# Kernel optimization log

Measured on AMD Instinct MI355X. Metric: run time of the kernel, lower is better.

Reference implementation:

```python
import jax, jax.numpy as jnp
import numpy as np

A = 9               # anchors per location (3 scales x 3 ratios)
STRIDE = 32         # backbone stride 16 * conv1 stride 2
PRE_NMS = 2000      # boxes kept before NMS
POST_NMS = 300      # rois kept after NMS
NMS_THRESH = 0.7
MIN_SIZE = 16.0
NEG = jnp.float32(-1e30)


def _generate_anchors(base_size=16, ratios=(0.5, 1.0, 2.0), scales=(8, 16, 32)):
    xc = yc = 0.5 * (base_size - 1)
    size = float(base_size * base_size)
    anchors = []
    for r in ratios:
        ws = np.round(np.sqrt(size / r))
        hs = np.round(ws * r)
        for s in scales:
            w, h = ws * s, hs * s
            anchors.append([xc - 0.5 * (w - 1), yc - 0.5 * (h - 1),
                            xc + 0.5 * (w - 1), yc + 0.5 * (h - 1)])
    return np.array(anchors, dtype=np.float32)  # [A,4]


def _conv(x, w, b, stride, pad):
    y = jax.lax.conv_general_dilated(
        x, w, (stride, stride), ((pad, pad), (pad, pad)),
        dimension_numbers=('NCHW', 'OIHW', 'NCHW'))
    return y + b[None, :, None, None]


def _iou_matrix(boxes):
    x1, y1, x2, y2 = boxes[:, 0], boxes[:, 1], boxes[:, 2], boxes[:, 3]
    area = (x2 - x1 + 1.0) * (y2 - y1 + 1.0)
    iw = jnp.maximum(0.0, jnp.minimum(x2[:, None], x2[None, :]) - jnp.maximum(x1[:, None], x1[None, :]) + 1.0)
    ih = jnp.maximum(0.0, jnp.minimum(y2[:, None], y2[None, :]) - jnp.maximum(y1[:, None], y1[None, :]) + 1.0)
    inter = iw * ih
    return inter / (area[:, None] + area[None, :] - inter)


def _nms_single(boxes, scores):
    # boxes [K,4] sorted by score desc; scores [K] (NEG = filtered out)
    K = boxes.shape[0]
    iou = _iou_matrix(boxes)
    prio = jnp.arange(K, 0, -1)

    def step(valid, _):
        any_valid = jnp.any(valid)
        pick = jnp.argmax(jnp.where(valid, prio, 0))
        new_valid = valid & (iou[pick] <= NMS_THRESH)
        return new_valid, (pick, any_valid)

    valid0 = scores > NEG * 0.5
    _, (picks, flags) = jax.lax.scan(step, valid0, None, length=POST_NMS)
    sel = boxes[picks] * flags[:, None].astype(boxes.dtype)
    return sel, jnp.sum(flags.astype(jnp.int32))


def _proposal(deltas, scores):
    B, _, H, W = deltas.shape
    im_h, im_w = float(H * STRIDE), float(W * STRIDE)
    anchors = jnp.asarray(_generate_anchors())  # [A,4]
    sx = (jnp.arange(W) * STRIDE).astype(jnp.float32)
    sy = (jnp.arange(H) * STRIDE).astype(jnp.float32)
    gx, gy = jnp.meshgrid(sx, sy)  # [H,W] each
    shift = jnp.stack([gx, gy, gx, gy], axis=-1)  # [H,W,4]
    anc = (shift[:, :, None, :] + anchors[None, None, :, :]).reshape(-1, 4)  # [H*W*A,4]

    d = deltas.reshape(B, A, 4, H, W).transpose(0, 3, 4, 1, 2).reshape(B, -1, 4)  # [B,N,4]
    s = scores[:, A:].transpose(0, 2, 3, 1).reshape(B, -1)  # fg scores [B,N]

    ws = anc[:, 2] - anc[:, 0] + 1.0
    hs = anc[:, 3] - anc[:, 1] + 1.0
    cx = anc[:, 0] + 0.5 * ws
    cy = anc[:, 1] + 0.5 * hs
    pcx = d[:, :, 0] * ws + cx
    pcy = d[:, :, 1] * hs + cy
    pw = jnp.exp(d[:, :, 2]) * ws
    ph = jnp.exp(d[:, :, 3]) * hs
    boxes = jnp.stack([pcx - 0.5 * pw, pcy - 0.5 * ph,
                       pcx + 0.5 * pw, pcy + 0.5 * ph], axis=-1)  # [B,N,4]
    lim = jnp.array([im_w - 1, im_h - 1, im_w - 1, im_h - 1], jnp.float32)
    boxes = jnp.minimum(jnp.maximum(boxes, 0.0), lim)

    bw = boxes[..., 2] - boxes[..., 0] + 1.0
    bh = boxes[..., 3] - boxes[..., 1] + 1.0
    s = jnp.where((bw >= MIN_SIZE) & (bh >= MIN_SIZE), s, NEG)

    top_s, idx = jax.lax.top_k(s, PRE_NMS)  # sorted desc
    top_b = jnp.take_along_axis(boxes, idx[:, :, None], axis=1)  # [B,PRE,4]

    sel, num = jax.vmap(_nms_single)(top_b, top_s)  # [B,POST,4], [B]
    bidx = jnp.broadcast_to(jnp.arange(B, dtype=sel.dtype)[:, None, None], (B, POST_NMS, 1))
    rois = jnp.concatenate([bidx, sel], axis=-1)  # [B,POST,5]
    return rois, num


def setup_inputs() -> dict:
    key = jax.random.key(0)
    k = jax.random.split(key, 4)
    x = jax.random.normal(k[0], (4, 512, 96, 160), jnp.float32)
    w1 = jax.random.normal(k[1], (512, 512, 3, 3), jnp.float32) * 0.02
    b1 = jnp.zeros((512,), jnp.float32)
    w_bbox = jax.random.normal(k[2], (36, 512, 1, 1), jnp.float32) * 0.02
    b_bbox = jnp.zeros((36,), jnp.float32)
    w_cls = jax.random.normal(k[3], (18, 512, 3, 3), jnp.float32) * 0.02
    b_cls = jnp.zeros((18,), jnp.float32)
    return dict(x=x, w1=w1, b1=b1, w_bbox=w_bbox, b_bbox=b_bbox, w_cls=w_cls, b_cls=b_cls)


def reference(x, w1, b1, w_bbox, b_bbox, w_cls, b_cls):
    feat = _conv(x, w1, b1, 2, 1)           # [B,512,H/2,W/2]
    deltas = _conv(feat, w_bbox, b_bbox, 1, 0)  # [B,36,h,w]
    cls = _conv(feat, w_cls, b_cls, 1, 1)       # [B,18,h,w]
    return _proposal(deltas, cls)
```

## Files before the change

kernel.cpp:

```cpp
#include <hip/hip_runtime.h>
#include <stdint.h>

typedef unsigned long long u64;
typedef unsigned int u32;

__constant__ float c_aw[9] = {184.f,368.f,736.f,128.f,256.f,512.f, 88.f,176.f,352.f};
__constant__ float c_ah[9] = { 96.f,192.f,384.f,128.f,256.f,512.f,176.f,352.f,704.f};

__global__ __launch_bounds__(256) void transpose_k(const float* __restrict__ w1,
                                                   float* __restrict__ wt2) {
  int e = blockIdx.x * 256 + threadIdx.x;
  int m = e & 7;
  int t = e >> 3;
  int k = t % 9;
  int r = t / 9;
  int ci = r & 511;
  int g = r >> 9;
  wt2[e] = w1[(size_t)(g * 8 + m) * 4608 + ci * 9 + k];
}

__global__ __launch_bounds__(256, 3) void conv1_k(const float* __restrict__ x,
                                                  const float* __restrict__ wt2,
                                                  const float* __restrict__ b1,
                                                  float* __restrict__ feat) {
  __shared__ float xs[8 * 9 * 164];
  const int tid = threadIdx.x;
  const int lane = tid & 63;
  const int wv = __builtin_amdgcn_readfirstlane(tid >> 6);
  const int owg = lane & 15;
  const int ohl = lane >> 4;
  const int n = blockIdx.z;
  const int gg = blockIdx.x * 4 + wv;
  const int oh0 = blockIdx.y * 4;
  const int ih_base = 2 * oh0 - 1;

  int soff[6], loff[6];
  float okf[6];
  bool act[6];
#pragma unroll
  for (int it = 0; it < 6; ++it) {
    int e2 = tid + 256 * it;
    act[it] = (e2 < 1449);
    int e = act[it] ? e2 : 0;
    int ih = e / 161;
    int c = e - ih * 161;
    int gih = ih_base + ih;
    int giw = c - 1;
    bool ok = act[it] && ((unsigned)gih < 96u) && ((unsigned)giw < 160u);
    int cg = min(max(gih, 0), 95);
    int cw = min(max(giw, 0), 159);
    soff[it] = cg * 160 + cw;
    loff[it] = ih * 164 + c;
    okf[it] = ok ? 1.f : 0.f;
  }

  float acc[8][5];
#pragma unroll
  for (int m = 0; m < 8; ++m)
#pragma unroll
    for (int j = 0; j < 5; ++j) acc[m][j] = 0.f;

  const float* xb = x + (size_t)n * 512 * 96 * 160;
  const float* wgb = wt2 + (size_t)gg * 512 * 72;

  float r[6][8];
#pragma unroll
  for (int it = 0; it < 6; ++it)
#pragma unroll
    for (int ci = 0; ci < 8; ++ci)
      r[it][ci] = xb[(size_t)ci * 15360 + soff[it]];

  for (int c0 = 0; c0 < 512; c0 += 8) {
    __syncthreads();
#pragma unroll
    for (int it = 0; it < 6; ++it) {
      if (act[it]) {
        const float m_ = okf[it];
#pragma unroll
        for (int ci = 0; ci < 8; ++ci)
          xs[loff[it] + ci * 1476] = m_ * r[it][ci];
      }
    }
    __syncthreads();
    if (c0 + 8 < 512) {
      const float* xn = xb + (size_t)(c0 + 8) * 15360;
#pragma unroll
      for (int it = 0; it < 6; ++it)
#pragma unroll
        for (int ci = 0; ci < 8; ++ci)
          r[it][ci] = xn[(size_t)ci * 15360 + soff[it]];
    }

    for (int ci = 0; ci < 8; ++ci) {
      const float* wp = wgb + (size_t)(c0 + ci) * 72;
      const float* xrow = &xs[(ci * 9 + 2 * ohl) * 164 + owg * 10];
#pragma unroll
      for (int kh = 0; kh < 3; ++kh) {
        float xv[12];
        const float* xr = xrow + kh * 164;
#pragma unroll
        for (int t2 = 0; t2 < 6; ++t2) {
          float2 t = *(const float2*)(xr + 2 * t2);
          xv[2 * t2] = t.x; xv[2 * t2 + 1] = t.y;
        }
#pragma unroll
        for (int kw = 0; kw < 3; ++kw) {
          const float* wk = wp + (kh * 3 + kw) * 8;
#pragma unroll
          for (int j = 0; j < 5; ++j) {
            const float xj = xv[kw + 2 * j];
            acc[0][j] += wk[0] * xj; acc[1][j] += wk[1] * xj;
            acc[2][j] += wk[2] * xj; acc[3][j] += wk[3] * xj;
            acc[4][j] += wk[4] * xj; acc[5][j] += wk[5] * xj;
            acc[6][j] += wk[6] * xj; acc[7][j] += wk[7] * xj;
          }
        }
      }
    }
  }
  const int oh = oh0 + ohl;
  const int owb = owg * 5;
#pragma unroll
  for (int m = 0; m < 8; ++m) {
    const int co = gg * 8 + m;
    const float bv = b1[co];
    float* op = &feat[(((size_t)n * 512 + co) * 48 + oh) * 80 + owb];
#pragma unroll
    for (int j = 0; j < 5; ++j) op[j] = acc[m][j] + bv;
  }
}

__global__ __launch_bounds__(256) void heads_k(const float* __restrict__ feat,
                                               const float* __restrict__ wb,
                                               const float* __restrict__ bb,
                                               const float* __restrict__ wcg,
                                               const float* __restrict__ bc,
                                               float* __restrict__ deltas,
                                               float* __restrict__ s) {
  __shared__ float smem[5328];
  const int tid = threadIdx.x;

  if (blockIdx.x < 120) {
    float* fs  = smem;
    float* wsb = smem + 2048;
    const int blk = blockIdx.x;
    const int b = blk / 30;
    const int pos0 = (blk % 30) * 128;
    const int pl = tid >> 1, cg = tid & 1;
    const int cbase = cg * 18;
    float acc[18];
#pragma unroll
    for (int j = 0; j < 18; ++j) acc[j] = 0.f;
    const float* fb = feat + (size_t)b * 512 * 3840;

    for (int c0 = 0; c0 < 512; c0 += 16) {
      for (int e = tid; e < 16 * 128; e += 256)
        fs[e] = fb[(size_t)(c0 + (e >> 7)) * 3840 + pos0 + (e & 127)];
      for (int e = tid; e < 16 * 36; e += 256) {
        int ci = e / 36, c = e - ci * 36;
        wsb[e] = wb[(size_t)c * 512 + c0 + ci];
      }
      __syncthreads();
      for (int ci = 0; ci < 16; ++ci) {
        float xv = fs[ci * 128 + pl];
#pragma unroll
        for (int j = 0; j < 18; ++j) acc[j] += xv * wsb[ci * 36 + cbase + j];
      }
      __syncthreads();
    }
    size_t o = ((size_t)b * 3840 + pos0 + pl) * 36 + cbase;
#pragma unroll
    for (int j = 0; j < 18; ++j) deltas[o + j] = acc[j] + bb[cbase + j];
  } else {
    float (*fs)[3][84] = (float(*)[3][84])smem;
    float (*wc)[9][9]  = (float(*)[9][9])(smem + 4032);
    const int bid2 = blockIdx.x - 120;
    const int oh = bid2 % 48;
    const int b = bid2 / 48;
    const int pos = tid % 80;
    const int cg = tid / 80;
    float acc[3] = {0.f, 0.f, 0.f};
    const float* fb = feat + (size_t)b * 512 * 3840;

    for (int c0 = 0; c0 < 512; c0 += 16) {
      for (int e = tid; e < 16 * 246; e += 256) {
        int ci = e / 246;
        int r = e - ci * 246;
        int ihl = r / 82;
        int iw = r - ihl * 82 - 1;
        int gih = oh - 1 + ihl;
        float v = 0.f;
        if ((unsigned)gih < 48u && (unsigned)iw < 80u)
          v = fb[(size_t)(c0 + ci) * 3840 + gih * 80 + iw];
        fs[ci][ihl][iw + 1] = v;
      }
      for (int e = tid; e < 16 * 81; e += 256) {
        int ci = e / 81;
        int r = e - ci * 81;
        int co = r / 9;
        int k = r - co * 9;
        wc[ci][co][k] = wcg[((size_t)(9 + co) * 512 + c0 + ci) * 9 + k];
      }
      __syncthreads();
      if (cg < 3) {
        const int cb = cg * 3;
        for (int ci = 0; ci < 16; ++ci) {
#pragma unroll
          for (int kh = 0; kh < 3; ++kh) {
#pragma unroll
            for (int kw = 0; kw < 3; ++kw) {
              float xv = fs[ci][kh][pos + kw];
              acc[0] += xv * wc[ci][cb + 0][kh * 3 + kw];
              acc[1] += xv * wc[ci][cb + 1][kh * 3 + kw];
              acc[2] += xv * wc[ci][cb + 2][kh * 3 + kw];
            }
          }
        }
      }
      __syncthreads();
    }
    if (cg < 3) {
      const int cb = cg * 3;
      size_t o = (size_t)b * 34560 + ((size_t)oh * 80 + pos) * 9 + cb;
#pragma unroll
      for (int j = 0; j < 3; ++j) s[o + j] = acc[j] + bc[9 + cb + j];
    }
  }
}

__global__ __launch_bounds__(256) void decode_k(const float* __restrict__ deltas,
                                                const float* __restrict__ s,
                                                float* __restrict__ boxes,
                                                u64* __restrict__ keys) {
  const int g = blockIdx.x * 256 + threadIdx.x;
  const int b = g / 34560;
  const int i = g - b * 34560;
  const int pos = i / 9;
  const int a = i - pos * 9;
  const int h = pos / 80;
  const int w = pos - h * 80;
  const float gx = (float)(w * 32);
  const float gy = (float)(h * 32);
  const float aw = c_aw[a], ah = c_ah[a];
  const float x1a = 7.5f - 0.5f * (aw - 1.f);
  const float y1a = 7.5f - 0.5f * (ah - 1.f);
  const float ws_ = aw, hs_ = ah;
  const float cx = (gx + x1a) + 0.5f * ws_;
  const float cy = (gy + y1a) + 0.5f * hs_;

  const float* dp = &deltas[((size_t)b * 3840 + pos) * 36 + a * 4];
  const float d0 = dp[0], d1 = dp[1], d2 = dp[2], d3 = dp[3];
  const float pcx = __fadd_rn(__fmul_rn(d0, ws_), cx);
  const float pcy = __fadd_rn(__fmul_rn(d1, hs_), cy);
  const float pw = __fmul_rn(expf(d2), ws_);
  const float ph = __fmul_rn(expf(d3), hs_);
  float bx1 = __fsub_rn(pcx, __fmul_rn(0.5f, pw));
  float by1 = __fsub_rn(pcy, __fmul_rn(0.5f, ph));
  float bx2 = __fadd_rn(pcx, __fmul_rn(0.5f, pw));
  float by2 = __fadd_rn(pcy, __fmul_rn(0.5f, ph));
  bx1 = fminf(fmaxf(bx1, 0.f), 2559.f);
  by1 = fminf(fmaxf(by1, 0.f), 1535.f);
  bx2 = fminf(fmaxf(bx2, 0.f), 2559.f);
  by2 = fminf(fmaxf(by2, 0.f), 1535.f);
  const float bw = __fadd_rn(__fsub_rn(bx2, bx1), 1.f);
  const float bh = __fadd_rn(__fsub_rn(by2, by1), 1.f);
  float sc = s[g];
  if (!(bw >= 16.f && bh >= 16.f)) sc = -1e30f;

  float4 bo;
  bo.x = bx1; bo.y = by1; bo.z = bx2; bo.w = by2;
  *(float4*)&boxes[(size_t)g * 4] = bo;

  u32 sb = __float_as_uint(sc);
  u32 ou = (sb & 0x80000000u) ? ~sb : (sb | 0x80000000u);
  keys[g] = ((u64)ou << 32) | (u32)(~(u32)i);
}

__global__ __launch_bounds__(1024) void selcomp_k(const u64* __restrict__ keys,
                                                  u64* __restrict__ sel) {
  __shared__ u32 h[2048];
  __shared__ int s_bin;
  __shared__ u32 s_above;
  __shared__ int sc;
  const int b = blockIdx.x;
  const int tid = threadIdx.x;
  const u64* kb = keys + (size_t)b * 34560;
  u64 prefix = 0, pmask = 0;
  int rank = 2000;

#pragma unroll 1
  for (int pass = 0; pass < 6; ++pass) {
    int shift = 53 - 11 * pass;
    if (shift < 0) shift = 0;
    h[tid] = 0; h[tid + 1024] = 0;
    __syncthreads();
    for (int i = tid; i < 34560; i += 1024) {
      u64 k = kb[i];
      if ((k & pmask) == prefix)
        atomicAdd(&h[(u32)((k >> shift) & 2047ull)], 1u);
    }
    __syncthreads();
    for (int off = 1; off < 2048; off <<= 1) {
      u32 t0, t1;
      { int i = tid;        t0 = h[i] + ((i + off < 2048) ? h[i + off] : 0u); }
      { int i = tid + 1024; t1 = h[i] + ((i + off < 2048) ? h[i + off] : 0u); }
      __syncthreads();
      h[tid] = t0; h[tid + 1024] = t1;
      __syncthreads();
    }
#pragma unroll
    for (int q = 0; q < 2; ++q) {
      int i = tid + 1024 * q;
      u32 Si = h[i];
      u32 Sn = (i < 2047) ? h[i + 1] : 0u;
      if ((int)Si >= rank && (int)Sn < rank) { s_bin = i; s_above = Sn; }
    }
    __syncthreads();
    rank -= (int)s_above;
    prefix |= ((u64)(u32)s_bin) << shift;
    pmask |= (2047ull << shift);
    __syncthreads();
  }
  if (tid == 0) sc = 0;
  __syncthreads();
  for (int i = tid; i < 34560; i += 1024) {
    u64 k = kb[i];
    if (k >= prefix) {
      int p = atomicAdd(&sc, 1);
      sel[(size_t)b * 2048 + p] = k;
    }
  }
}

__global__ __launch_bounds__(1024) void nms2_k(const u64* __restrict__ sel,
                                               const float* __restrict__ boxes,
                                               float* __restrict__ out) {
  __shared__ u64 K[2048];
  __shared__ float bx1[2000], by1[2000], bx2[2000], by2[2000], ar[2000];
  __shared__ unsigned char val[2000];
  __shared__ int s_pick, s_cur, s_cnt;
  const int b = blockIdx.x;
  const int tid = threadIdx.x;

  for (int i = tid; i < 2048; i += 1024)
    K[i] = (i < 2000) ? sel[(size_t)b * 2048 + i] : 0ull;
  __syncthreads();
  for (int k2 = 2; k2 <= 2048; k2 <<= 1) {
    for (int j = k2 >> 1; j > 0; j >>= 1) {
      for (int i = tid; i < 2048; i += 1024) {
        int l = i ^ j;
        if (l > i) {
          u64 a = K[i], c = K[l];
          bool up = ((i & k2) == 0);
          if (up ? (a < c) : (a > c)) { K[i] = c; K[l] = a; }
        }
      }
      __syncthreads();
    }
  }
  for (int i = tid; i < 2000; i += 1024) {
    u64 key = K[i];
    u32 ou = (u32)(key >> 32);
    int idx = (int)(~(u32)key);
    u32 sb = (ou & 0x80000000u) ? (ou & 0x7FFFFFFFu) : ~ou;
    float sc = __uint_as_float(sb);
    const float4 bo = *(const float4*)&boxes[((size_t)b * 34560 + idx) * 4];
    bx1[i] = bo.x; by1[i] = bo.y; bx2[i] = bo.z; by2[i] = bo.w;
    ar[i] = __fmul_rn(__fadd_rn(__fsub_rn(bo.z, bo.x), 1.f),
                      __fadd_rn(__fsub_rn(bo.w, bo.y), 1.f));
    val[i] = (sc > -5e29f) ? 1 : 0;
  }
  if (tid == 0) { s_cur = 0; s_cnt = 0; }
  __syncthreads();

  for (int t = 0; t < 300; ++t) {
    if (tid == 0) {
      int c = s_cur;
      while (c < 2000 && !val[c]) ++c;
      if (c < 2000) { s_pick = c; s_cur = c + 1; s_cnt = t + 1; }
      else s_pick = -1;
    }
    __syncthreads();
    const int p = s_pick;
    if (p < 0) break;
    const float px1 = bx1[p], py1 = by1[p], px2 = bx2[p], py2 = by2[p], pa = ar[p];
    if (tid == 0) {
      float* row = out + ((size_t)b * 300 + t) * 5;
      row[0] = (float)b; row[1] = px1; row[2] = py1; row[3] = px2; row[4] = py2;
    }
    for (int jj = p + 1 + tid; jj < 2000; jj += 1024) {
      if (val[jj]) {
        float iw = __fadd_rn(__fsub_rn(fminf(px2, bx2[jj]), fmaxf(px1, bx1[jj])), 1.f);
        iw = fmaxf(0.f, iw);
        float ih = __fadd_rn(__fsub_rn(fminf(py2, by2[jj]), fmaxf(py1, by1[jj])), 1.f);
        ih = fmaxf(0.f, ih);
        float inter = __fmul_rn(iw, ih);
        float denom = __fsub_rn(__fadd_rn(pa, ar[jj]), inter);
        float iou = __fdiv_rn(inter, denom);
        if (iou > 0.7f) val[jj] = 0;
      }
    }
    __syncthreads();
  }

  __syncthreads();
  const int cnt = s_cnt;
  for (int t = cnt + tid; t < 300; t += 1024) {
    float* row = out + ((size_t)b * 300 + t) * 5;
    row[0] = (float)b; row[1] = 0.f; row[2] = 0.f; row[3] = 0.f; row[4] = 0.f;
  }
  if (tid == 0) out[6000 + b] = (float)cnt;
}

extern "C" void kernel_launch(void* const* d_in, const int* in_sizes, int n_in,
                              void* d_out, int out_size, void* d_ws, size_t ws_size,
                              hipStream_t stream) {
  const float* x  = (const float*)d_in[0];
  const float* w1 = (const float*)d_in[1];
  const float* b1 = (const float*)d_in[2];
  const float* wb = (const float*)d_in[3];
  const float* bb = (const float*)d_in[4];
  const float* wc = (const float*)d_in[5];
  const float* bc = (const float*)d_in[6];
  float* out = (float*)d_out;
  char* ws = (char*)d_ws;

  float* feat   = (float*)(ws + 0);
  float* wt2    = (float*)(ws + 31457280);
  float* deltas = (float*)(ws + 40894464);
  float* s      = (float*)(ws + 43106304);
  float* boxes  = (float*)(ws + 43659264);
  u64*   keys   = (u64*)  (ws + 45871104);
  u64*   sel    = (u64*)  (ws + 46977088);

  hipLaunchKernelGGL(transpose_k, dim3(9216), dim3(256), 0, stream, w1, wt2);
  hipLaunchKernelGGL(conv1_k, dim3(16, 12, 4), dim3(256), 0, stream, x, wt2, b1, feat);
  hipLaunchKernelGGL(heads_k, dim3(312), dim3(256), 0, stream, feat, wb, bb, wc, bc, deltas, s);
  hipLaunchKernelGGL(decode_k, dim3(540), dim3(256), 0, stream, deltas, s, boxes, keys);
  hipLaunchKernelGGL(selcomp_k, dim3(4), dim3(1024), 0, stream, keys, sel);
  hipLaunchKernelGGL(nms2_k, dim3(4), dim3(1024), 0, stream, sel, boxes, out);
}
```

Before: 1.599 ms.

## Double-buffer conv1 LDS tile, privatize selection histograms, shrink NMS block

The conv1 kernel now uses two LDS buffers of 4 input channels each instead of one 8-channel buffer. This lets the next tile be written while the current one is computed, so one barrier per iteration can go. The weight transpose switches to coalesced reads with scattered writes. The radix-select histogram is replicated four ways to cut atomic contention, with an extra reduction step added. The NMS kernel drops from 1024 to 256 threads per block to reduce barrier cost in its serial 300-step loop. The risk is that it also loses parallelism in the bitonic sort and the IoU sweep.

```diff
diff --git a/kernel.cpp b/kernel.cpp
--- a/kernel.cpp
+++ b/kernel.cpp
@@ -10,20 +10,19 @@
 __global__ __launch_bounds__(256) void transpose_k(const float* __restrict__ w1,
                                                    float* __restrict__ wt2) {
   int e = blockIdx.x * 256 + threadIdx.x;
-  int m = e & 7;
-  int t = e >> 3;
-  int k = t % 9;
-  int r = t / 9;
-  int ci = r & 511;
-  int g = r >> 9;
-  wt2[e] = w1[(size_t)(g * 8 + m) * 4608 + ci * 9 + k];
+  int q = e % 4608;
+  int co = e / 4608;
+  int ci = q / 9;
+  int k = q - ci * 9;
+  int g = co >> 3, m = co & 7;
+  wt2[(((size_t)g * 512 + ci) * 9 + k) * 8 + m] = w1[e];
 }
 
 __global__ __launch_bounds__(256, 3) void conv1_k(const float* __restrict__ x,
                                                   const float* __restrict__ wt2,
                                                   const float* __restrict__ b1,
                                                   float* __restrict__ feat) {
-  __shared__ float xs[8 * 9 * 164];
+  __shared__ float xs[2][4 * 9 * 164];
   const int tid = threadIdx.x;
   const int lane = tid & 63;
   const int wv = __builtin_amdgcn_readfirstlane(tid >> 6);
@@ -47,9 +46,7 @@
     int gih = ih_base + ih;
     int giw = c - 1;
     bool ok = act[it] && ((unsigned)gih < 96u) && ((unsigned)giw < 160u);
-    int cg = min(max(gih, 0), 95);
-    int cw = min(max(giw, 0), 159);
-    soff[it] = cg * 160 + cw;
+    soff[it] = min(max(gih, 0), 95) * 160 + min(max(giw, 0), 159);
     loff[it] = ih * 164 + c;
     okf[it] = ok ? 1.f : 0.f;
   }
@@ -63,45 +60,62 @@
   const float* xb = x + (size_t)n * 512 * 96 * 160;
   const float* wgb = wt2 + (size_t)gg * 512 * 72;
 
-  float r[6][8];
+  float r[6][4];
 #pragma unroll
   for (int it = 0; it < 6; ++it)
 #pragma unroll
-    for (int ci = 0; ci < 8; ++ci)
+    for (int ci = 0; ci < 4; ++ci)
       r[it][ci] = xb[(size_t)ci * 15360 + soff[it]];
-
-  for (int c0 = 0; c0 < 512; c0 += 8) {
-    __syncthreads();
-#pragma unroll
-    for (int it = 0; it < 6; ++it) {
-      if (act[it]) {
-        const float m_ = okf[it];
-#pragma unroll
-        for (int ci = 0; ci < 8; ++ci)
-          xs[loff[it] + ci * 1476] = m_ * r[it][ci];
-      }
-    }
-    __syncthreads();
-    if (c0 + 8 < 512) {
-      const float* xn = xb + (size_t)(c0 + 8) * 15360;
+#pragma unroll
+  for (int it = 0; it < 6; ++it) {
+    if (act[it]) {
+      const float m_ = okf[it];
+#pragma unroll
+      for (int ci = 0; ci < 4; ++ci)
+        xs[0][loff[it] + ci * 1476] = m_ * r[it][ci];
+    }
+  }
+#pragma unroll
+  for (int it = 0; it < 6; ++it)
+#pragma unroll
+    for (int ci = 0; ci < 4; ++ci)
+      r[it][ci] = xb[(size_t)(4 + ci) * 15360 + soff[it]];
+
+  for (int t = 0; t < 128; ++t) {
+    __syncthreads();
+    const int cur = t & 1;
+    if (t < 127) {
+#pragma unroll
+      for (int it = 0; it < 6; ++it) {
+        if (act[it]) {
+          const float m_ = okf[it];
+#pragma unroll
+          for (int ci = 0; ci < 4; ++ci)
+            xs[cur ^ 1][loff[it] + ci * 1476] = m_ * r[it][ci];
+        }
+      }
+    }
+    if (t < 126) {
+      const float* xn = xb + (size_t)(t + 2) * 4 * 15360;
 #pragma unroll
       for (int it = 0; it < 6; ++it)
 #pragma unroll
-        for (int ci = 0; ci < 8; ++ci)
+        for (int ci = 0; ci < 4; ++ci)
           r[it][ci] = xn[(size_t)ci * 15360 + soff[it]];
     }
 
-    for (int ci = 0; ci < 8; ++ci) {
+    const int c0 = t * 4;
+    for (int ci = 0; ci < 4; ++ci) {
       const float* wp = wgb + (size_t)(c0 + ci) * 72;
-      const float* xrow = &xs[(ci * 9 + 2 * ohl) * 164 + owg * 10];
+      const float* xrow = &xs[cur][(ci * 9 + 2 * ohl) * 164 + owg * 10];
 #pragma unroll
       for (int kh = 0; kh < 3; ++kh) {
         float xv[12];
         const float* xr = xrow + kh * 164;
 #pragma unroll
         for (int t2 = 0; t2 < 6; ++t2) {
-          float2 t = *(const float2*)(xr + 2 * t2);
-          xv[2 * t2] = t.x; xv[2 * t2 + 1] = t.y;
+          float2 tt = *(const float2*)(xr + 2 * t2);
+          xv[2 * t2] = tt.x; xv[2 * t2 + 1] = tt.y;
         }
 #pragma unroll
         for (int kw = 0; kw < 3; ++kw) {
@@ -278,7 +292,7 @@
 
 __global__ __launch_bounds__(1024) void selcomp_k(const u64* __restrict__ keys,
                                                   u64* __restrict__ sel) {
-  __shared__ u32 h[2048];
+  __shared__ u32 h4[4 * 2048];
   __shared__ int s_bin;
   __shared__ u32 s_above;
   __shared__ int sc;
@@ -287,32 +301,41 @@
   const u64* kb = keys + (size_t)b * 34560;
   u64 prefix = 0, pmask = 0;
   int rank = 2000;
+  const int rep = (tid & 3) * 2048;
 
 #pragma unroll 1
   for (int pass = 0; pass < 6; ++pass) {
     int shift = 53 - 11 * pass;
     if (shift < 0) shift = 0;
-    h[tid] = 0; h[tid + 1024] = 0;
+#pragma unroll
+    for (int q = 0; q < 8; ++q) h4[tid + 1024 * q] = 0;
     __syncthreads();
     for (int i = tid; i < 34560; i += 1024) {
       u64 k = kb[i];
       if ((k & pmask) == prefix)
-        atomicAdd(&h[(u32)((k >> shift) & 2047ull)], 1u);
+        atomicAdd(&h4[rep + (u32)((k >> shift) & 2047ull)], 1u);
+    }
+    __syncthreads();
+    {
+      int i = tid;
+      if (i < 2048) h4[i] += h4[i + 2048] + h4[i + 4096] + h4[i + 6144];
+      i = tid + 1024;
+      if (i < 2048) h4[i] += h4[i + 2048] + h4[i + 4096] + h4[i + 6144];
     }
     __syncthreads();
     for (int off = 1; off < 2048; off <<= 1) {
       u32 t0, t1;
-      { int i = tid;        t0 = h[i] + ((i + off < 2048) ? h[i + off] : 0u); }
-      { int i = tid + 1024; t1 = h[i] + ((i + off < 2048) ? h[i + off] : 0u); }
-      __syncthreads();
-      h[tid] = t0; h[tid + 1024] = t1;
+      { int i = tid;        t0 = h4[i] + ((i + off < 2048) ? h4[i + off] : 0u); }
+      { int i = tid + 1024; t1 = h4[i] + ((i + off < 2048) ? h4[i + off] : 0u); }
+      __syncthreads();
+      h4[tid] = t0; h4[tid + 1024] = t1;
       __syncthreads();
     }
 #pragma unroll
     for (int q = 0; q < 2; ++q) {
       int i = tid + 1024 * q;
-      u32 Si = h[i];
-      u32 Sn = (i < 2047) ? h[i + 1] : 0u;
+      u32 Si = h4[i];
+      u32 Sn = (i < 2047) ? h4[i + 1] : 0u;
       if ((int)Si >= rank && (int)Sn < rank) { s_bin = i; s_above = Sn; }
     }
     __syncthreads();
@@ -332,9 +355,9 @@
   }
 }
 
-__global__ __launch_bounds__(1024) void nms2_k(const u64* __restrict__ sel,
-                                               const float* __restrict__ boxes,
-                                               float* __restrict__ out) {
+__global__ __launch_bounds__(256) void nms2_k(const u64* __restrict__ sel,
+                                              const float* __restrict__ boxes,
+                                              float* __restrict__ out) {
   __shared__ u64 K[2048];
   __shared__ float bx1[2000], by1[2000], bx2[2000], by2[2000], ar[2000];
   __shared__ unsigned char val[2000];
@@ -342,12 +365,12 @@
   const int b = blockIdx.x;
   const int tid = threadIdx.x;
 
-  for (int i = tid; i < 2048; i += 1024)
+  for (int i = tid; i < 2048; i += 256)
     K[i] = (i < 2000) ? sel[(size_t)b * 2048 + i] : 0ull;
   __syncthreads();
   for (int k2 = 2; k2 <= 2048; k2 <<= 1) {
     for (int j = k2 >> 1; j > 0; j >>= 1) {
-      for (int i = tid; i < 2048; i += 1024) {
+      for (int i = tid; i < 2048; i += 256) {
         int l = i ^ j;
         if (l > i) {
           u64 a = K[i], c = K[l];
@@ -358,7 +381,7 @@
       __syncthreads();
     }
   }
-  for (int i = tid; i < 2000; i += 1024) {
+  for (int i = tid; i < 2000; i += 256) {
     u64 key = K[i];
     u32 ou = (u32)(key >> 32);
     int idx = (int)(~(u32)key);
@@ -388,7 +411,7 @@
       float* row = out + ((size_t)b * 300 + t) * 5;
       row[0] = (float)b; row[1] = px1; row[2] = py1; row[3] = px2; row[4] = py2;
     }
-    for (int jj = p + 1 + tid; jj < 2000; jj += 1024) {
+    for (int jj = p + 1 + tid; jj < 2000; jj += 256) {
       if (val[jj]) {
         float iw = __fadd_rn(__fsub_rn(fminf(px2, bx2[jj]), fmaxf(px1, bx1[jj])), 1.f);
         iw = fmaxf(0.f, iw);
@@ -405,7 +428,7 @@
 
   __syncthreads();
   const int cnt = s_cnt;
-  for (int t = cnt + tid; t < 300; t += 1024) {
+  for (int t = cnt + tid; t < 300; t += 256) {
     float* row = out + ((size_t)b * 300 + t) * 5;
     row[0] = (float)b; row[1] = 0.f; row[2] = 0.f; row[3] = 0.f; row[4] = 0.f;
   }
@@ -438,5 +461,5 @@
   hipLaunchKernelGGL(heads_k, dim3(312), dim3(256), 0, stream, feat, wb, bb, wc, bc, deltas, s);
   hipLaunchKernelGGL(decode_k, dim3(540), dim3(256), 0, stream, deltas, s, boxes, keys);
   hipLaunchKernelGGL(selcomp_k, dim3(4), dim3(1024), 0, stream, keys, sel);
-  hipLaunchKernelGGL(nms2_k, dim3(4), dim3(1024), 0, stream, sel, boxes, out);
-}
+  hipLaunchKernelGGL(nms2_k, dim3(4), dim3(256), 0, stream, sel, boxes, out);
+}
```

Result: slower. 1.994 ms (+24.7%).
